# Optimization experiments

Hardware: AMD Instinct MI355X
Metric: run time of the kernel (lower is better)

Reference implementation:

```python
import jax, jax.numpy as jnp
import numpy as np

D_IN, D_HEAD, D_EXPAND, D_OUT, H = 512, 64, 2048, 512, 8
D_Q = D_HEAD * H  # 512
D_K = D_HEAD * H  # 512
D_V = D_IN * H    # 4096 (non-standard: per-head value dim = d_in)
EPS = 1e-5


def layernorm(x, g, b):
    mu = jnp.mean(x, axis=-1, keepdims=True)
    var = jnp.mean(jnp.square(x - mu), axis=-1, keepdims=True)
    return (x - mu) * jax.lax.rsqrt(var + EPS) * g + b


def setup_inputs() -> dict:
    key = jax.random.key(0)
    ks = jax.random.split(key, 12)
    B, N = 2, 2048
    s_in = 1.0 / np.sqrt(D_IN)
    s_mh = 1.0 / np.sqrt(D_IN * H)
    s_ex = 1.0 / np.sqrt(D_EXPAND)
    return {
        "x": jax.random.normal(ks[0], (B, N, D_IN), jnp.float32),
        "ln1_g": jnp.ones((D_IN,), jnp.float32),
        "ln1_b": jnp.zeros((D_IN,), jnp.float32),
        "Wqkv": jax.random.normal(ks[1], (D_IN, D_Q + D_K + D_V), jnp.float32) * s_in,
        "bqkv": jax.random.normal(ks[2], (D_Q + D_K + D_V,), jnp.float32) * 0.01,
        "Wm": jax.random.normal(ks[3], (D_IN * H, D_IN), jnp.float32) * s_mh,
        "bm": jax.random.normal(ks[4], (D_IN,), jnp.float32) * 0.01,
        "ln2_g": jnp.ones((D_IN,), jnp.float32),
        "ln2_b": jnp.zeros((D_IN,), jnp.float32),
        "W1": jax.random.normal(ks[5], (D_IN, D_EXPAND), jnp.float32) * s_in,
        "b1": jax.random.normal(ks[6], (D_EXPAND,), jnp.float32) * 0.01,
        "W2": jax.random.normal(ks[7], (D_EXPAND, D_OUT), jnp.float32) * s_ex,
        "b2": jax.random.normal(ks[8], (D_OUT,), jnp.float32) * 0.01,
    }


def reference(x, ln1_g, ln1_b, Wqkv, bqkv, Wm, bm, ln2_g, ln2_b, W1, b1, W2, b2):
    B, N, _ = x.shape
    scale = D_HEAD ** -0.5
    qkv = layernorm(x, ln1_g, ln1_b) @ Wqkv + bqkv
    q, k, v = jnp.split(qkv, [D_Q, D_Q + D_K], axis=-1)
    q = q.reshape(B, N, H, D_HEAD).transpose(0, 2, 1, 3)  # (B,H,N,dh)
    k = k.reshape(B, N, H, D_HEAD).transpose(0, 2, 1, 3)
    v = v.reshape(B, N, H, D_IN).transpose(0, 2, 1, 3)    # (B,H,N,d_in)
    attn = jax.nn.softmax(jnp.einsum('bhnd,bhmd->bhnm', q, k) * scale, axis=-1)
    out = jnp.einsum('bhnm,bhmc->bhnc', attn, v)          # (B,H,N,d_in)
    out = out.transpose(0, 2, 1, 3).reshape(B, N, H * D_IN)
    x2 = x + out @ Wm + bm
    h = layernorm(x2, ln2_g, ln2_b) @ W1 + b1
    h = h * jax.nn.sigmoid(h)  # Swish
    return h @ W2 + b2 + x2    # shortcut = Identity (d_in == d_out)
```

## Files before the change

### kernel.cpp

```cpp
#include <hip/hip_runtime.h>
#include <cmath>

typedef unsigned short u16;
typedef unsigned int   u32;
typedef __attribute__((ext_vector_type(8))) __bf16 bf16x8;
typedef __attribute__((ext_vector_type(4))) float  f32x4;
typedef __attribute__((ext_vector_type(8))) unsigned short u16x8;
typedef __attribute__((ext_vector_type(4))) unsigned short u16x4;

#define DEV __device__ __forceinline__

DEV float bf2f(u16 u){ union{u32 i; float f;} v; v.i=((u32)u)<<16; return v.f; }
DEV u16 f2bf(float f){ union{float f; u32 i;} v; v.f=f; u32 r=v.i+0x7fffu+((v.i>>16)&1u); return (u16)(r>>16); }

#if defined(__has_builtin) && __has_builtin(__builtin_amdgcn_global_load_lds)
DEV void gld16(const void* g, void* l){
  __builtin_amdgcn_global_load_lds((__attribute__((address_space(1))) void*)g,
                                   (__attribute__((address_space(3))) void*)l, 16, 0, 0);
}
#else
DEV void gld16(const void* g, void* l){ *(u16x8*)l = *(const u16x8*)g; }
#endif

#if defined(__has_builtin) && __has_builtin(__builtin_amdgcn_exp2f)
DEV float fexp2(float x){ return __builtin_amdgcn_exp2f(x); }
#else
DEV float fexp2(float x){ return exp2f(x); }
#endif

__global__ void detect_k(const u16* __restrict__ x, int* __restrict__ flag)
{
  if (threadIdx.x == 0 && blockIdx.x == 0){
    int sane = 0;
    for (int i = 0; i < 64; ++i){
      int e = (x[i] >> 7) & 0xFF;
      sane += (e >= 100 && e <= 150);
    }
    *flag = (sane < 56) ? 1 : 0;
  }
}

__global__ __launch_bounds__(256)
void conv_vecs(const void* a0,const void* a1,const void* a2,const void* a3,
               const void* a4,const void* a5,const void* a6,const void* a7,
               float* __restrict__ dst, const int* __restrict__ flag)
{
  int i = blockIdx.x*256 + threadIdx.x;
  if (i >= 10240) return;
  const void* src; int off;
  if      (i < 512)  { src=a0; off=i; }
  else if (i < 1024) { src=a1; off=i-512; }
  else if (i < 6144) { src=a2; off=i-1024; }
  else if (i < 6656) { src=a3; off=i-6144; }
  else if (i < 7168) { src=a4; off=i-6656; }
  else if (i < 7680) { src=a5; off=i-7168; }
  else if (i < 9728) { src=a6; off=i-7680; }
  else               { src=a7; off=i-9728; }
  dst[i] = (*flag) ? ((const float*)src)[off] : bf2f(((const u16*)src)[off]);
}

#define SWZ_SRC(c) (((c)&7) ^ (((c)>>3)&7))

template<int SWZ>
DEV void remap_xcd(int& bx, int& by)
{
  if (SWZ==1){
    int L = by*(int)gridDim.x + bx;
    int xcd = L & 7, l = L >> 3;
    int chunk = (int)gridDim.x >> 3;
    bx = xcd*chunk + (l % chunk);
    by = l / chunk;
  } else if (SWZ==2){
    int L = by*(int)gridDim.x + bx;
    int xcd = L & 7, l = L >> 3;
    int chunk = (int)gridDim.y >> 3;
    by = xcd*chunk + (l % chunk);
    bx = l / chunk;
  }
}

template<int MODE, int SWZ, bool VT>
__global__ __launch_bounds__(512)
void gemm_bt(const u16* __restrict__ A, const u16* __restrict__ BT,
             void* __restrict__ C, const float* __restrict__ bias,
             int K, int lda, int ldb, int ldc, u16* __restrict__ vout)
{
  __shared__ u16 AB[4*128*64];
  u16* As0 = AB;
  u16* Bs0 = AB + 2*128*64;
  const int tid  = threadIdx.x;
  const int lane = tid & 63;
  const int quad = lane>>4, l7 = lane&7, l15 = lane&15;
  const int wv   = tid >> 6;
  const int wm   = wv >> 2, wn = wv & 3;
  int bx = blockIdx.x, by = blockIdx.y;
  remap_xcd<SWZ>(bx, by);
  const long m0 = (long)by * 128;
  const long n0 = (long)bx * 128;

  f32x4 acc[4][2];
#pragma unroll
  for (int i=0;i<4;i++)
#pragma unroll
    for (int j=0;j<2;j++) acc[i][j] = (f32x4){0.f,0.f,0.f,0.f};

  auto stage = [&](int bi, int k0){
#pragma unroll
    for (int i=0;i<2;i++){
      int c = i*512 + tid;
      gld16(A  + (m0 + (c>>3))*lda + k0 + SWZ_SRC(c)*8, &As0[bi*8192 + c*8]);
      gld16(BT + (n0 + (c>>3))*ldb + k0 + SWZ_SRC(c)*8, &Bs0[bi*8192 + c*8]);
    }
  };

  const int S = K >> 6;
  stage(0, 0);
  __syncthreads();

  for (int s=0; s<S; ++s){
    const int cb = s & 1;
    if (s+1 < S) stage(cb^1, (s+1)<<6);
#pragma unroll
    for (int kk=0;kk<2;kk++){
      const int ch = ((kk*4 + quad) ^ l7) * 8;
      bf16x8 af[4], bfr[2];
#pragma unroll
      for (int t=0;t<4;t++)
        af[t]  = *(const bf16x8*)&As0[cb*8192 + (wm*64 + t*16 + l15)*64 + ch];
#pragma unroll
      for (int t=0;t<2;t++)
        bfr[t] = *(const bf16x8*)&Bs0[cb*8192 + (wn*32 + t*16 + l15)*64 + ch];
#pragma unroll
      for (int ti=0;ti<4;ti++)
#pragma unroll
        for (int tj=0;tj<2;tj++)
          acc[ti][tj] = __builtin_amdgcn_mfma_f32_16x16x32_bf16(af[ti], bfr[tj], acc[ti][tj], 0,0,0);
    }
    __syncthreads();
  }

  if (VT && n0 >= 1024){
    const int hh   = (int)((n0 - 1024) >> 9);
    const int c0   = (int)((n0 - 1024) & 511);
    const int b_   = (int)(m0 >> 11);
    const int kloc = (int)(m0 & 2047);
    u16* vb = vout + ((long)(b_*8 + hh))*512*2048 + kloc;
    u16* Ts = AB;
#pragma unroll
    for (int ti=0;ti<4;ti++)
#pragma unroll
    for (int tj=0;tj<2;tj++)
#pragma unroll
    for (int r=0;r<4;r++){
      int row = wm*64 + ti*16 + quad*4 + r;
      int cl  = wn*32 + tj*16 + l15;
      Ts[row*132 + cl] = f2bf(acc[ti][tj][r] + bias[n0 + cl]);
    }
    __syncthreads();
#pragma unroll
    for (int step=0; step<4; ++step){
      int cr = step*32 + (tid>>4);
      int t8 = (tid&15)*8;
      u16x8 pk;
#pragma unroll
      for (int j=0;j<8;j++) pk[j] = Ts[(t8+j)*132 + cr];
      *(u16x8*)(vb + (long)(c0 + cr)*2048 + t8) = pk;
    }
    return;
  }

#pragma unroll
  for (int ti=0;ti<4;ti++)
#pragma unroll
  for (int tj=0;tj<2;tj++)
#pragma unroll
  for (int r=0;r<4;r++){
    long row = m0 + wm*64 + ti*16 + quad*4 + r;
    long col = n0 + wn*32 + tj*16 + l15;
    float v = acc[ti][tj][r] + bias[col];
    if (MODE==2) v = v / (1.f + __expf(-v));
    ((u16*)C)[row*ldc+col] = f2bf(v);
  }
}

template<int MODE, int SWZ>
__global__ __launch_bounds__(512)
void gemm_n64(const u16* __restrict__ A, const u16* __restrict__ BT,
              void* __restrict__ C, const float* __restrict__ bias,
              const void* __restrict__ res,
              int K, int lda, int ldb, int ldc, const int* __restrict__ flag)
{
  __shared__ u16 As[2][128*64];
  __shared__ u16 Bs[2][64*64];
  const int tid  = threadIdx.x;
  const int lane = tid & 63;
  const int quad = lane>>4, l7 = lane&7, l15 = lane&15;
  const int wm   = tid >> 6;
  int bx = blockIdx.x, by = blockIdx.y;
  remap_xcd<SWZ>(bx, by);
  const long m0 = (long)by * 128;
  const long n0 = (long)bx * 64;
  const bool f32io = flag && (*flag != 0);

  f32x4 acc[4];
#pragma unroll
  for (int j=0;j<4;j++) acc[j] = (f32x4){0.f,0.f,0.f,0.f};

  auto stage = [&](int bi, int k0){
#pragma unroll
    for (int i=0;i<2;i++){
      int c = i*512 + tid;
      gld16(A + (m0 + (c>>3))*lda + k0 + SWZ_SRC(c)*8, &As[bi][c*8]);
    }
    { int c = tid;
      gld16(BT + (n0 + (c>>3))*ldb + k0 + SWZ_SRC(c)*8, &Bs[bi][c*8]); }
  };

  const int S = K >> 6;
  stage(0, 0);
  __syncthreads();

  for (int s=0; s<S; ++s){
    const int cb = s & 1;
    if (s+1 < S) stage(cb^1, (s+1)<<6);
#pragma unroll
    for (int kk=0;kk<2;kk++){
      const int ch = ((kk*4 + quad) ^ l7) * 8;
      bf16x8 af = *(const bf16x8*)&As[cb][(wm*16 + l15)*64 + ch];
      bf16x8 bfr[4];
#pragma unroll
      for (int t=0;t<4;t++)
        bfr[t] = *(const bf16x8*)&Bs[cb][(t*16 + l15)*64 + ch];
#pragma unroll
      for (int tj=0;tj<4;tj++)
        acc[tj] = __builtin_amdgcn_mfma_f32_16x16x32_bf16(af, bfr[tj], acc[tj], 0,0,0);
    }
    __syncthreads();
  }

#pragma unroll
  for (int tj=0;tj<4;tj++)
#pragma unroll
  for (int r=0;r<4;r++){
    long row = m0 + wm*16 + quad*4 + r;
    long col = n0 + tj*16 + l15;
    float v = acc[tj][r] + bias[col];
    if (MODE==1){
      v += f32io ? ((const float*)res)[row*ldc+col]
                 : bf2f(((const u16*)res)[row*ldc+col]);
      ((float*)C)[row*ldc+col] = v;
    } else {
      v += ((const float*)res)[row*ldc+col];
      if (f32io) ((float*)C)[row*ldc+col] = v;
      else       ((u16*)C)[row*ldc+col]   = f2bf(v);
    }
  }
}

__global__ __launch_bounds__(512, 2)
void att_flash(const u16* __restrict__ qkv, const u16* __restrict__ vt,
               u16* __restrict__ ao)
{
  __shared__ u16 Qs[128*64];
  __shared__ u16 Ks[2][64*64];
  __shared__ u16 Ps[128*68];
  __shared__ u16 Vs[512*64];
  __shared__ float m_run[128], l_run[128], alph[128];
  __shared__ int resc[2];
  const int tid=threadIdx.x, lane=tid&63, wv=tid>>6;
  const int wm=wv>>2, wn=wv&3;
  const int quad=lane>>4, l7=lane&7, l15=lane&15;
  const int bid = blockIdx.x;
  const int id  = ((bid&7)<<5) + (bid>>3);
  const int qt  = id & 15, bh = id >> 4;
  const int b = bh>>3, h = bh&7;
  const long q0 = (long)qt*128;
  const u16* qb = qkv + ((long)b*2048 + q0)*5120 + h*64;
  const u16* kb = qkv + (long)b*2048*5120 + 512 + h*64;
  const u16* vb = vt + (long)bh*512*2048;

#pragma unroll
  for (int i=0;i<2;i++){
    int c=i*512+tid;
    gld16(qb + (long)(c>>3)*5120 + SWZ_SRC(c)*8, &Qs[c*8]);
  }
  { int c=tid; gld16(kb + (long)(c>>3)*5120 + SWZ_SRC(c)*8, &Ks[0][c*8]); }
  if (tid<128){ m_run[tid] = -1e30f; l_run[tid] = 0.f; }
  if (tid==0){ resc[0]=0; resc[1]=0; }

  f32x4 o[4][8];
#pragma unroll
  for (int i=0;i<4;i++)
#pragma unroll
    for (int j=0;j<8;j++) o[i][j] = (f32x4){0.f,0.f,0.f,0.f};

  __syncthreads();
  bf16x8 qreg[2];
#pragma unroll
  for (int kk=0;kk<2;kk++)
    qreg[kk] = *(const bf16x8*)&Qs[(wv*16 + l15)*64 + ((kk*4 + quad) ^ l7)*8];

  for (int mt=0; mt<32; ++mt){
    const long m0 = (long)mt*64;
    const int cur = mt&1;
    __syncthreads();

    if (mt < 31){ int c=tid; gld16(kb + (m0+64 + (c>>3))*5120 + SWZ_SRC(c)*8, &Ks[cur^1][c*8]); }
#pragma unroll
    for (int i=0;i<8;i++){
      int c=i*512+tid;
      gld16(vb + (long)(c>>3)*2048 + m0 + SWZ_SRC(c)*8, &Vs[c*8]);
    }
    if (tid==0) resc[cur^1] = 0;

    f32x4 s[4];
#pragma unroll
    for (int j=0;j<4;j++) s[j] = (f32x4){0.f,0.f,0.f,0.f};
#pragma unroll
    for (int kk=0;kk<2;kk++){
      const int ch = ((kk*4 + quad) ^ l7) * 8;
#pragma unroll
      for (int tj=0;tj<4;tj++){
        bf16x8 bfr = *(const bf16x8*)&Ks[cur][(tj*16 + l15)*64 + ch];
        s[tj] = __builtin_amdgcn_mfma_f32_16x16x32_bf16(qreg[kk], bfr, s[tj], 0,0,0);
      }
    }

    float nm[4], al[4], rs[4];
    bool chg = false;
#pragma unroll
    for (int r=0;r<4;r++){
      float vm = fmaxf(fmaxf(s[0][r],s[1][r]), fmaxf(s[2][r],s[3][r]));
      vm = fmaxf(vm, __shfl_xor(vm,1)); vm = fmaxf(vm, __shfl_xor(vm,2));
      vm = fmaxf(vm, __shfl_xor(vm,4)); vm = fmaxf(vm, __shfl_xor(vm,8));
      float mo = m_run[wv*16 + quad*4 + r];
      float vs = vm*0.125f;
      bool c_ = (vs > mo + 8.f);
      nm[r] = c_ ? vs : mo;
      al[r] = c_ ? __expf(mo - vs) : 1.f;
      chg |= c_;
      rs[r] = 0.f;
    }
    float nml[4];
#pragma unroll
    for (int r=0;r<4;r++) nml[r] = nm[r]*1.44269504f;
#pragma unroll
    for (int tj=0;tj<4;tj++)
#pragma unroll
    for (int r=0;r<4;r++){
      float pv = fexp2(fmaf(s[tj][r], 0.18033688f, -nml[r]));
      rs[r] += pv;
      Ps[(wv*16 + quad*4 + r)*68 + tj*16 + l15] = f2bf(pv);
    }
#pragma unroll
    for (int r=0;r<4;r++){
      rs[r] += __shfl_xor(rs[r],1); rs[r] += __shfl_xor(rs[r],2);
      rs[r] += __shfl_xor(rs[r],4); rs[r] += __shfl_xor(rs[r],8);
    }
    if (l15==0){
#pragma unroll
      for (int r=0;r<4;r++){
        int row = wv*16 + quad*4 + r;
        alph[row]  = al[r];
        m_run[row] = nm[r];
        l_run[row] = l_run[row]*al[r] + rs[r];
      }
    }
    if (__any((int)chg) && lane==0) resc[cur] = 1;
    __syncthreads();

    if (resc[cur]){
      float a_[4][4];
#pragma unroll
      for (int ti=0;ti<4;ti++)
#pragma unroll
        for (int r=0;r<4;r++) a_[ti][r] = alph[wm*64 + ti*16 + quad*4 + r];
#pragma unroll
      for (int ti=0;ti<4;ti++)
#pragma unroll
      for (int tj=0;tj<8;tj++)
#pragma unroll
        for (int r=0;r<4;r++) o[ti][tj][r] *= a_[ti][r];
    }
#pragma unroll
    for (int kk=0;kk<2;kk++){
      const int ch = ((kk*4 + quad) ^ l7) * 8;
      bf16x8 af[4], bfr[8];
#pragma unroll
      for (int t=0;t<4;t++){
        int base = (wm*64 + t*16 + l15)*68 + kk*32 + quad*8;
        union { u16x4 hh[2]; bf16x8 v; } u;
        u.hh[0] = *(const u16x4*)&Ps[base];
        u.hh[1] = *(const u16x4*)&Ps[base+4];
        af[t] = u.v;
      }
#pragma unroll
      for (int t=0;t<8;t++)
        bfr[t] = *(const bf16x8*)&Vs[(wn*128 + t*16 + l15)*64 + ch];
#pragma unroll
      for (int ti=0;ti<4;ti++)
#pragma unroll
        for (int tj=0;tj<8;tj++)
          o[ti][tj] = __builtin_amdgcn_mfma_f32_16x16x32_bf16(af[ti], bfr[tj], o[ti][tj], 0,0,0);
    }
  }

  float rl[4][4];
#pragma unroll
  for (int ti=0;ti<4;ti++)
#pragma unroll
    for (int r=0;r<4;r++) rl[ti][r] = 1.f / l_run[wm*64 + ti*16 + quad*4 + r];
#pragma unroll
  for (int ti=0;ti<4;ti++)
#pragma unroll
  for (int tj=0;tj<8;tj++)
#pragma unroll
  for (int r=0;r<4;r++){
    long rown = q0 + wm*64 + ti*16 + quad*4 + r;
    long col  = wn*128 + tj*16 + l15;
    ao[((long)b*2048 + rown)*4096 + (long)h*512 + col] = f2bf(o[ti][tj][r]*rl[ti][r]);
  }
}

template<int SRC>
__global__ __launch_bounds__(256)
void ln_kernel(const void* __restrict__ xin, const float* __restrict__ g,
               const float* __restrict__ bb, u16* __restrict__ out,
               const int* __restrict__ flag)
{
  const int tid=threadIdx.x, lane=tid&63, wv=tid>>6;
  const long row = (long)blockIdx.x*4 + wv;
  const bool f32 = (SRC==1) || (flag && *flag != 0);
  float v[8];
  if (f32){
    const float* xr = (const float*)xin + row*512 + lane*8;
#pragma unroll
    for (int j=0;j<8;j++) v[j]=xr[j];
  } else {
    const u16* xr = (const u16*)xin + row*512 + lane*8;
    u16x8 xv = *(const u16x8*)xr;
#pragma unroll
    for (int j=0;j<8;j++) v[j]=bf2f(xv[j]);
  }
  float s1=0.f, s2=0.f;
#pragma unroll
  for (int j=0;j<8;j++){ s1+=v[j]; s2+=v[j]*v[j]; }
  for (int off=1; off<64; off<<=1){ s1+=__shfl_xor(s1,off); s2+=__shfl_xor(s2,off); }
  float mu  = s1*(1.f/512.f);
  float var = s2*(1.f/512.f) - mu*mu;
  float rs  = rsqrtf(var + 1e-5f);
  u16x8 ov;
#pragma unroll
  for (int j=0;j<8;j++){
    int col = lane*8+j;
    ov[j] = f2bf((v[j]-mu)*rs*g[col] + bb[col]);
  }
  *(u16x8*)(out + row*512 + lane*8) = ov;
}

template<bool DUAL>
__global__ __launch_bounds__(256)
void transpose_k(const void* __restrict__ in_, u16* __restrict__ out,
                 int ldi, int ldo, long izh, long izl, long oz,
                 const int* __restrict__ flag)
{
  __shared__ u16 t[32][33];
  const int z = blockIdx.z;
  const bool f32 = DUAL && flag && (*flag != 0);
  const long zoff = (long)(z>>3)*izh + (long)(z&7)*izl;
  out += (long)z*oz;
  const int tx = threadIdx.x, ty = threadIdx.y;
  const long c  = (long)blockIdx.x*32 + tx;
  const long r0 = (long)blockIdx.y*32;
  if (f32){
    const float* in = (const float*)in_ + zoff;
#pragma unroll
    for (int j=0;j<4;j++) t[ty+j*8][tx] = f2bf(in[(r0+ty+j*8)*ldi + c]);
  } else {
    const u16* in = (const u16*)in_ + zoff;
#pragma unroll
    for (int j=0;j<4;j++) t[ty+j*8][tx] = in[(r0+ty+j*8)*ldi + c];
  }
  __syncthreads();
  const long rr = r0 + tx;
  const long cc = (long)blockIdx.x*32 + ty;
#pragma unroll
  for (int j=0;j<4;j++) out[(cc+j*8)*ldo + rr] = t[tx][ty+j*8];
}

extern "C" void kernel_launch(void* const* d_in, const int* in_sizes, int n_in,
                              void* d_out, int out_size, void* d_ws, size_t ws_size,
                              hipStream_t stream)
{
  const void* x    = d_in[0];
  const void* ln1g = d_in[1];
  const void* ln1b = d_in[2];
  const void* Wqkv = d_in[3];
  const void* bqkv = d_in[4];
  const void* Wm   = d_in[5];
  const void* bm   = d_in[6];
  const void* ln2g = d_in[7];
  const void* ln2b = d_in[8];
  const void* W1   = d_in[9];
  const void* b1   = d_in[10];
  const void* W2   = d_in[11];
  const void* b2   = d_in[12];

  char* p = (char*)d_ws;
  auto take = [&](size_t n){ void* r=(void*)p; p += (n + 255) & ~(size_t)255; return r; };
  u16*   lnb   = (u16*)  take((size_t)4096*512*2);
  u16*   qkv   = (u16*)  take((size_t)4096*5120*2);
  u16*   vtb   = (u16*)  take((size_t)16*512*2048*2);
  u16*   wqkvT = (u16*)  take((size_t)5120*512*2);
  u16*   wmT   = (u16*)  take((size_t)512*4096*2);
  u16*   w1T   = (u16*)  take((size_t)2048*512*2);
  u16*   w2T   = (u16*)  take((size_t)512*2048*2);
  u16*   ao    = (u16*)  take((size_t)4096*4096*2);
  float* cvec  = (float*)take((size_t)10240*4);
  int*   flag  = (int*)  take(4);
  float* x2    = (float*)vtb;
  u16*   hb    = qkv;

  detect_k<<<1, 64, 0, stream>>>((const u16*)x, flag);
  conv_vecs<<<40, 256, 0, stream>>>(ln1g, ln1b, bqkv, bm, ln2g, ln2b, b1, b2, cvec, flag);

  dim3 tb(32,8);
  transpose_k<true><<<dim3(160,16,1), tb, 0, stream>>>(Wqkv, wqkvT, 5120, 512, 0,0,0, flag);
  transpose_k<true><<<dim3(16,128,1), tb, 0, stream>>>(Wm,   wmT,   512, 4096, 0,0,0, flag);
  transpose_k<true><<<dim3(64,16,1),  tb, 0, stream>>>(W1,   w1T,  2048, 512, 0,0,0, flag);
  transpose_k<true><<<dim3(16,64,1),  tb, 0, stream>>>(W2,   w2T,   512, 2048, 0,0,0, flag);

  ln_kernel<0><<<1024, 256, 0, stream>>>(x, cvec+0, cvec+512, lnb, flag);
  gemm_bt<0,1,true><<<dim3(40,32), 512, 0, stream>>>(lnb, wqkvT, qkv, cvec+1024,
                                                     512, 512, 512, 5120, vtb);

  att_flash<<<dim3(256), 512, 0, stream>>>(qkv, vtb, ao);

  gemm_n64<1,2><<<dim3(8,32), 512, 0, stream>>>(ao, wmT, x2, cvec+6144, x,
                                                4096, 4096, 4096, 512, flag);
  ln_kernel<1><<<1024, 256, 0, stream>>>(x2, cvec+6656, cvec+7168, lnb, nullptr);
  gemm_bt<2,2,false><<<dim3(16,32), 512, 0, stream>>>(lnb, w1T, hb, cvec+7680,
                                                      512, 512, 512, 2048, nullptr);
  gemm_n64<3,2><<<dim3(8,32), 512, 0, stream>>>(hb, w2T, d_out, cvec+9728, x2,
                                                2048, 2048, 2048, 512, flag);
}
```

Baseline: 359.1 us.

## Use per-wave running max and compute softmax row sums with MFMA

```diff
diff --git a/kernel.cpp b/kernel.cpp
--- a/kernel.cpp
+++ b/kernel.cpp
@@ -265,7 +265,8 @@
   __shared__ u16 Ks[2][64*64];
   __shared__ u16 Ps[128*68];
   __shared__ u16 Vs[512*64];
-  __shared__ float m_run[128], l_run[128], alph[128];
+  __shared__ float alph[8];
+  __shared__ float l_lds[128];
   __shared__ int resc[2];
   const int tid=threadIdx.x, lane=tid&63, wv=tid>>6;
   const int wm=wv>>2, wn=wv&3;
@@ -285,14 +286,22 @@
     gld16(qb + (long)(c>>3)*5120 + SWZ_SRC(c)*8, &Qs[c*8]);
   }
   { int c=tid; gld16(kb + (long)(c>>3)*5120 + SWZ_SRC(c)*8, &Ks[0][c*8]); }
-  if (tid<128){ m_run[tid] = -1e30f; l_run[tid] = 0.f; }
   if (tid==0){ resc[0]=0; resc[1]=0; }
 
+  union { u16x8 u; bf16x8 v; } one_u;
+#pragma unroll
+  for (int j=0;j<8;j++) one_u.u[j] = 0x3F80;
+  const bf16x8 ones = one_u.v;
+
   f32x4 o[4][8];
 #pragma unroll
   for (int i=0;i<4;i++)
 #pragma unroll
     for (int j=0;j<8;j++) o[i][j] = (f32x4){0.f,0.f,0.f,0.f};
+  f32x4 ol[4];
+#pragma unroll
+  for (int i=0;i<4;i++) ol[i] = (f32x4){0.f,0.f,0.f,0.f};
+  float m_w = -1e30f;
 
   __syncthreads();
   bf16x8 qreg[2];
@@ -326,61 +335,46 @@
       }
     }
 
-    float nm[4], al[4], rs[4];
-    bool chg = false;
+    float vm = s[0][0];
+#pragma unroll
+    for (int tj=0;tj<4;tj++)
+#pragma unroll
+      for (int r=0;r<4;r++) vm = fmaxf(vm, s[tj][r]);
+    vm = fmaxf(vm, __shfl_xor(vm,1));  vm = fmaxf(vm, __shfl_xor(vm,2));
+    vm = fmaxf(vm, __shfl_xor(vm,4));  vm = fmaxf(vm, __shfl_xor(vm,8));
+    vm = fmaxf(vm, __shfl_xor(vm,16)); vm = fmaxf(vm, __shfl_xor(vm,32));
+    const float vs = vm*0.125f;
+    const bool c_ = (vs > m_w + 8.f);
+    const float nm = c_ ? vs : m_w;
+    const float al = c_ ? __expf(m_w - nm) : 1.f;
+    m_w = nm;
+    const float nml = nm*1.44269504f;
+#pragma unroll
+    for (int tj=0;tj<4;tj++)
 #pragma unroll
     for (int r=0;r<4;r++){
-      float vm = fmaxf(fmaxf(s[0][r],s[1][r]), fmaxf(s[2][r],s[3][r]));
-      vm = fmaxf(vm, __shfl_xor(vm,1)); vm = fmaxf(vm, __shfl_xor(vm,2));
-      vm = fmaxf(vm, __shfl_xor(vm,4)); vm = fmaxf(vm, __shfl_xor(vm,8));
-      float mo = m_run[wv*16 + quad*4 + r];
-      float vs = vm*0.125f;
-      bool c_ = (vs > mo + 8.f);
-      nm[r] = c_ ? vs : mo;
-      al[r] = c_ ? __expf(mo - vs) : 1.f;
-      chg |= c_;
-      rs[r] = 0.f;
-    }
-    float nml[4];
-#pragma unroll
-    for (int r=0;r<4;r++) nml[r] = nm[r]*1.44269504f;
-#pragma unroll
-    for (int tj=0;tj<4;tj++)
-#pragma unroll
-    for (int r=0;r<4;r++){
-      float pv = fexp2(fmaf(s[tj][r], 0.18033688f, -nml[r]));
-      rs[r] += pv;
+      float pv = fexp2(fmaf(s[tj][r], 0.18033688f, -nml));
       Ps[(wv*16 + quad*4 + r)*68 + tj*16 + l15] = f2bf(pv);
     }
-#pragma unroll
-    for (int r=0;r<4;r++){
-      rs[r] += __shfl_xor(rs[r],1); rs[r] += __shfl_xor(rs[r],2);
-      rs[r] += __shfl_xor(rs[r],4); rs[r] += __shfl_xor(rs[r],8);
-    }
-    if (l15==0){
-#pragma unroll
-      for (int r=0;r<4;r++){
-        int row = wv*16 + quad*4 + r;
-        alph[row]  = al[r];
-        m_run[row] = nm[r];
-        l_run[row] = l_run[row]*al[r] + rs[r];
+    if (lane==0){ alph[wv] = al; if (c_) resc[cur] = 1; }
+    __syncthreads();
+
+    if (resc[cur]){
+      float a_[4];
+#pragma unroll
+      for (int ti=0;ti<4;ti++) a_[ti] = alph[wm*4 + ti];
+#pragma unroll
+      for (int ti=0;ti<4;ti++)
+#pragma unroll
+      for (int tj=0;tj<8;tj++)
+#pragma unroll
+        for (int r=0;r<4;r++) o[ti][tj][r] *= a_[ti];
+      if (wn==0){
+#pragma unroll
+        for (int ti=0;ti<4;ti++)
+#pragma unroll
+          for (int r=0;r<4;r++) ol[ti][r] *= a_[ti];
       }
-    }
-    if (__any((int)chg) && lane==0) resc[cur] = 1;
-    __syncthreads();
-
-    if (resc[cur]){
-      float a_[4][4];
-#pragma unroll
-      for (int ti=0;ti<4;ti++)
-#pragma unroll
-        for (int r=0;r<4;r++) a_[ti][r] = alph[wm*64 + ti*16 + quad*4 + r];
-#pragma unroll
-      for (int ti=0;ti<4;ti++)
-#pragma unroll
-      for (int tj=0;tj<8;tj++)
-#pragma unroll
-        for (int r=0;r<4;r++) o[ti][tj][r] *= a_[ti][r];
     }
 #pragma unroll
     for (int kk=0;kk<2;kk++){
@@ -402,14 +396,26 @@
 #pragma unroll
         for (int tj=0;tj<8;tj++)
           o[ti][tj] = __builtin_amdgcn_mfma_f32_16x16x32_bf16(af[ti], bfr[tj], o[ti][tj], 0,0,0);
-    }
-  }
-
+      if (wn==0){
+#pragma unroll
+        for (int ti=0;ti<4;ti++)
+          ol[ti] = __builtin_amdgcn_mfma_f32_16x16x32_bf16(af[ti], ones, ol[ti], 0,0,0);
+      }
+    }
+  }
+
+  if (wn==0 && l15==0){
+#pragma unroll
+    for (int ti=0;ti<4;ti++)
+#pragma unroll
+      for (int r=0;r<4;r++) l_lds[wm*64 + ti*16 + quad*4 + r] = ol[ti][r];
+  }
+  __syncthreads();
   float rl[4][4];
 #pragma unroll
   for (int ti=0;ti<4;ti++)
 #pragma unroll
-    for (int r=0;r<4;r++) rl[ti][r] = 1.f / l_run[wm*64 + ti*16 + quad*4 + r];
+    for (int r=0;r<4;r++) rl[ti][r] = 1.f / l_lds[wm*64 + ti*16 + quad*4 + r];
 #pragma unroll
   for (int ti=0;ti<4;ti++)
 #pragma unroll
```

Result: no change. 359.1 us (-0.0%).
